# Kernel optimization log

Measured on AMD Instinct MI355X. Metric: run time of the kernel, lower is better.

Reference implementation:

```python
import jax, jax.numpy as jnp
import numpy as np

B, N, H, W = 2, 65536, 256, 256
FEA, OUT, CMP, MAX_PT = 8, 512, 32, 64
EPS = 1e-5


def _xavier(key, fan_in, fan_out):
    scale = np.sqrt(2.0 / (fan_in + fan_out)).astype(np.float32)
    return jax.random.normal(key, (fan_in, fan_out), dtype=jnp.float32) * scale


def setup_inputs() -> dict:
    key = jax.random.key(0)
    ks = jax.random.split(key, 8)
    pt_fea = jax.random.normal(ks[0], (B, N, FEA), dtype=jnp.float32)
    xy_ind = jax.random.randint(ks[1], (B, N, 2), 0, H, dtype=jnp.int32)
    return {
        "pt_fea": pt_fea,
        "bn0_g": jnp.ones((FEA,), jnp.float32), "bn0_b": jnp.zeros((FEA,), jnp.float32),
        "W1": _xavier(ks[2], FEA, 64),
        "bn1_g": jnp.ones((64,), jnp.float32), "bn1_b": jnp.zeros((64,), jnp.float32),
        "W2": _xavier(ks[3], 64, 128),
        "bn2_g": jnp.ones((128,), jnp.float32), "bn2_b": jnp.zeros((128,), jnp.float32),
        "W3": _xavier(ks[4], 128, 256),
        "bn3_g": jnp.ones((256,), jnp.float32), "bn3_b": jnp.zeros((256,), jnp.float32),
        "W4": _xavier(ks[5], 256, OUT),
        "Wc": _xavier(ks[6], OUT, CMP),
        "xy_ind": xy_ind,
    }


def _forward(pt_fea, bn0_g, bn0_b, W1, bn1_g, bn1_b, W2, bn2_g, bn2_b,
             W3, bn3_g, bn3_b, W4, Wc, xy_ind):
    Bc, Nc, Fc = pt_fea.shape
    P = Bc * Nc
    feats = pt_fea.reshape(P, Fc)
    batch_id = jnp.repeat(jnp.arange(Bc, dtype=jnp.int32), Nc)
    xy = xy_ind.reshape(P, 2)
    keys = batch_id * (H * W) + xy[:, 0] * W + xy[:, 1]  # linearized voxel id

    # random shuffle of points (torch.randperm)
    perm = jax.random.permutation(jax.random.key(42), P)
    feats = feats[perm]
    keys = keys[perm]

    # rank of each point within its voxel, in shuffled order
    # (== grp_range_torch(unq_cnt)[argsort(argsort(unq_inv))])
    order = jnp.argsort(keys)  # stable
    sk = keys[order]
    pos = jnp.arange(P)
    new_grp = jnp.concatenate([jnp.array([True]), sk[1:] != sk[:-1]])
    grp_start = jax.lax.cummax(jnp.where(new_grp, pos, 0))
    rank = jnp.zeros(P, jnp.int32).at[order].set((pos - grp_start).astype(jnp.int32))
    mask = rank < MAX_PT  # keep at most MAX_PT points per voxel

    # PPmodel: BN -> Lin -> BN -> ReLU x3 -> Lin, BN stats over kept points only
    m = mask[:, None].astype(feats.dtype)
    cnt = jnp.sum(m)

    def bn(x, g, b):
        mu = jnp.sum(x * m, axis=0) / cnt
        var = jnp.sum(jnp.square(x - mu) * m, axis=0) / cnt  # biased var
        return (x - mu) * jax.lax.rsqrt(var + EPS) * g + b

    x = bn(feats, bn0_g, bn0_b)
    x = jax.nn.relu(bn(x @ W1, bn1_g, bn1_b))
    x = jax.nn.relu(bn(x @ W2, bn2_g, bn2_b))
    x = jax.nn.relu(bn(x @ W3, bn3_g, bn3_b))
    x = x @ W4  # [P, OUT]

    # scatter_max segment reduction into dense voxel grid
    NEG = jnp.finfo(x.dtype).min
    x = jnp.where(mask[:, None], x, NEG)
    S = Bc * H * W
    pooled = jax.ops.segment_max(x, keys, num_segments=S)
    occupied = jax.ops.segment_sum(jnp.ones(P, x.dtype), keys, num_segments=S) > 0
    pooled = jnp.where(occupied[:, None], pooled, 0.0)

    comp = jax.nn.relu(pooled @ Wc)  # fea_compression
    comp = jnp.where(occupied[:, None], comp, 0.0)  # empty voxels stay zero
    out = comp.reshape(Bc, H, W, CMP).transpose(0, 3, 1, 2)  # [B, C, H, W]
    return out


def reference(pt_fea, bn0_g, bn0_b, W1, bn1_g, bn1_b, W2, bn2_g, bn2_b,
              W3, bn3_g, bn3_b, W4, Wc, xy_ind):
    return _forward(pt_fea, bn0_g, bn0_b, W1, bn1_g, bn1_b, W2, bn2_g, bn2_b,
                    W3, bn3_g, bn3_b, W4, Wc, xy_ind)
```

## Files before the change

kernel.cpp:

```cpp
#include <hip/hip_runtime.h>
#include <cstdint>
#include <cstddef>


#define P_TOT  131072
#define HWSZ   65536
#define WGRID  256
#define S_TOT  131072
#define EPS    1e-5f
#define CNTF   131072.0f

#define OFF_Y3    0ull
#define OFF_Y1    67108864ull
#define OFF_Y2    100663296ull
#define OFF_POOL  67108864ull
#define OFF_CNT   201326592ull
#define OFF_ST    201850880ull
#define OFF_OFFS  201916416ull
#define OFF_CUR   202440704ull
#define OFF_BSUM  202964992ull
#define OFF_PIDF  202969088ull
#define OFF_SEND  203493376ull
#define OFF_SKEY  204017664ull
#define OFF_INV   204541952ull
#define OFF_W3F   205066240ull
#define OFF_W4F   205131776ull
#define OFF_WCF   205393920ull
#define OFF_W2F   205426688ull
#define OFF_SCSH  205443072ull

typedef __attribute__((ext_vector_type(8)))  short bf16x8;
typedef __attribute__((ext_vector_type(16))) float f32x16;

__device__ __forceinline__ unsigned f2bf(float f) {
    unsigned u = __float_as_uint(f);
    return (u + 0x7FFFu + ((u >> 16) & 1u)) >> 16;
}
__device__ __forceinline__ float bf2f(unsigned h) {
    return __uint_as_float(h << 16);
}

__global__ __launch_bounds__(256) void k_zero(uint4* __restrict__ p, int n_u4) {
    int i = blockIdx.x * blockDim.x + threadIdx.x;
    if (i < n_u4) p[i] = make_uint4(0u, 0u, 0u, 0u);
}

__global__ __launch_bounds__(256) void k_prepw(
    const float* __restrict__ W2, const float* __restrict__ W3,
    const float* __restrict__ W4, const float* __restrict__ Wc,
    uint4* __restrict__ W2F, uint4* __restrict__ W3F,
    uint4* __restrict__ W4F, uint4* __restrict__ WcF)
{
    int gw = (blockIdx.x * 256 + threadIdx.x) >> 6;
    int l = threadIdx.x & 63;
    const float* W; uint4* dst; int M, mt, ks, fi;
    if (gw < 64)       { fi = gw;       W = W3; dst = W3F; M = 256; mt = fi >> 3; ks = fi & 7;  }
    else if (gw < 320) { fi = gw - 64;  W = W4; dst = W4F; M = 512; mt = fi >> 4; ks = fi & 15; }
    else if (gw < 352) { fi = gw - 320; W = Wc; dst = WcF; M = 32;  mt = 0;      ks = fi;      }
    else               { fi = gw - 352; W = W2; dst = W2F; M = 128; mt = fi >> 2; ks = fi & 3;  }
    int m = mt * 32 + (l & 31);
    int k0 = ks * 16 + (l >> 5) * 8;
    unsigned p[4];
    #pragma unroll
    for (int jj = 0; jj < 4; ++jj) {
        unsigned lo = f2bf(W[(size_t)(k0 + 2*jj)     * M + m]);
        unsigned hi = f2bf(W[(size_t)(k0 + 2*jj + 1) * M + m]);
        p[jj] = lo | (hi << 16);
    }
    dst[(size_t)fi * 64 + l] = make_uint4(p[0], p[1], p[2], p[3]);
}

__global__ __launch_bounds__(256) void k_bnprep(
    const float* __restrict__ st, const float* __restrict__ g,
    const float* __restrict__ b, float* __restrict__ sc,
    float* __restrict__ sh, int nch)
{
    int c = blockIdx.x * 256 + threadIdx.x;
    if (c >= nch) return;
    float mu = st[c * 16] * (1.0f / CNTF);
    float var = st[(nch + c) * 16] * (1.0f / CNTF) - mu * mu;
    float rs = rsqrtf(var + EPS);
    float s = rs * g[c];
    sc[c] = s;
    sh[c] = b[c] - mu * s;
}

__global__ __launch_bounds__(256) void k_fold(
    unsigned short* __restrict__ y, const float* __restrict__ sc,
    const float* __restrict__ sh, int nch, int n_u4)
{
    int i = blockIdx.x * 256 + threadIdx.x;
    if (i >= n_u4) return;
    int ch0 = (i * 8) & (nch - 1);
    float4 s0 = *(const float4*)(sc + ch0), s1 = *(const float4*)(sc + ch0 + 4);
    float4 h0 = *(const float4*)(sh + ch0), h1 = *(const float4*)(sh + ch0 + 4);
    float scv[8] = {s0.x,s0.y,s0.z,s0.w,s1.x,s1.y,s1.z,s1.w};
    float shv[8] = {h0.x,h0.y,h0.z,h0.w,h1.x,h1.y,h1.z,h1.w};
    uint4 e = ((const uint4*)y)[i];
    unsigned eu[4] = {e.x, e.y, e.z, e.w};
    unsigned ou[4];
    #pragma unroll
    for (int jj = 0; jj < 4; ++jj) {
        float x0 = fmaxf(fmaf(bf2f(eu[jj] & 0xFFFFu), scv[2*jj],   shv[2*jj]),   0.f);
        float x1 = fmaxf(fmaf(bf2f(eu[jj] >> 16),     scv[2*jj+1], shv[2*jj+1]), 0.f);
        ou[jj] = f2bf(x0) | (f2bf(x1) << 16);
    }
    ((uint4*)y)[i] = make_uint4(ou[0], ou[1], ou[2], ou[3]);
}

__global__ __launch_bounds__(256) void k_foldf(
    unsigned short* __restrict__ y, const float* __restrict__ sc,
    const float* __restrict__ sh, int n_u4)
{
    int i = blockIdx.x * 256 + threadIdx.x;
    if (i >= n_u4) return;
    int ch0 = ((i >> 6) & 15) * 16 + ((i >> 5) & 1) * 8;
    float4 s0 = *(const float4*)(sc + ch0), s1 = *(const float4*)(sc + ch0 + 4);
    float4 h0 = *(const float4*)(sh + ch0), h1 = *(const float4*)(sh + ch0 + 4);
    float scv[8] = {s0.x,s0.y,s0.z,s0.w,s1.x,s1.y,s1.z,s1.w};
    float shv[8] = {h0.x,h0.y,h0.z,h0.w,h1.x,h1.y,h1.z,h1.w};
    uint4 e = ((const uint4*)y)[i];
    unsigned eu[4] = {e.x, e.y, e.z, e.w};
    unsigned ou[4];
    #pragma unroll
    for (int jj = 0; jj < 4; ++jj) {
        float x0 = fmaxf(fmaf(bf2f(eu[jj] & 0xFFFFu), scv[2*jj],   shv[2*jj]),   0.f);
        float x1 = fmaxf(fmaf(bf2f(eu[jj] >> 16),     scv[2*jj+1], shv[2*jj+1]), 0.f);
        ou[jj] = f2bf(x0) | (f2bf(x1) << 16);
    }
    ((uint4*)y)[i] = make_uint4(ou[0], ou[1], ou[2], ou[3]);
}

__global__ __launch_bounds__(256) void k_stats0(
    const float* __restrict__ pt, const int* __restrict__ xy,
    float* __restrict__ st0, unsigned* __restrict__ counts)
{
    __shared__ float part[4][16];
    const int tid = threadIdx.x;
    const int p = blockIdx.x * 256 + tid;
    const float4* f4 = (const float4*)(pt + (size_t)p * 8);
    float4 a = f4[0], b = f4[1];
    float v[8] = {a.x,a.y,a.z,a.w,b.x,b.y,b.z,b.w};
    int key = (p >> 16) * HWSZ + xy[2*p] * WGRID + xy[2*p + 1];
    atomicAdd(&counts[key], 1u);
    float s[8], q[8];
    #pragma unroll
    for (int k = 0; k < 8; ++k) { s[k] = v[k]; q[k] = v[k]*v[k]; }
    #pragma unroll
    for (int k = 0; k < 8; ++k) {
        #pragma unroll
        for (int off = 32; off > 0; off >>= 1) {
            s[k] += __shfl_down(s[k], off);
            q[k] += __shfl_down(q[k], off);
        }
    }
    if ((tid & 63) == 0) {
        int w = tid >> 6;
        #pragma unroll
        for (int k = 0; k < 8; ++k) { part[w][k] = s[k]; part[w][8 + k] = q[k]; }
    }
    __syncthreads();
    if (tid < 16) {
        float t = part[0][tid] + part[1][tid] + part[2][tid] + part[3][tid];
        atomicAdd(&st0[tid * 16], t);
    }
}

__global__ __launch_bounds__(256) void k_lin1(
    const float* __restrict__ pt, const float* __restrict__ g0,
    const float* __restrict__ b0, const float* __restrict__ W1,
    const float* __restrict__ st0, float* __restrict__ y1,
    float* __restrict__ st1)
{
    __shared__ float x0s[64 * 8];
    __shared__ float w1s[8 * 64];
    __shared__ float sc0s[8], sh0s[8];
    __shared__ float red[256];
    const int tid = threadIdx.x;

    if (tid < 8) {
        float mu = st0[tid * 16] * (1.0f / CNTF);
        float var = st0[(8 + tid) * 16] * (1.0f / CNTF) - mu * mu;
        float rs = rsqrtf(var + EPS);
        sc0s[tid] = rs * g0[tid];
        sh0s[tid] = b0[tid] - mu * rs * g0[tid];
    }
    if (tid < 128) ((float4*)w1s)[tid] = ((const float4*)W1)[tid];
    const int c = tid & 63;
    const int psub = tid >> 6;
    float ssum = 0.f, ssq = 0.f;
    for (int t = 0; t < 4; ++t) {
        const int pbase = blockIdx.x * 256 + t * 64;
        __syncthreads();
        if (tid < 128) {
            float4 f = ((const float4*)(pt + (size_t)pbase * 8))[tid];
            int cc = (tid & 1) * 4;
            f.x = fmaf(f.x, sc0s[cc + 0], sh0s[cc + 0]);
            f.y = fmaf(f.y, sc0s[cc + 1], sh0s[cc + 1]);
            f.z = fmaf(f.z, sc0s[cc + 2], sh0s[cc + 2]);
            f.w = fmaf(f.w, sc0s[cc + 3], sh0s[cc + 3]);
            ((float4*)x0s)[tid] = f;
        }
        __syncthreads();
        #pragma unroll
        for (int i = 0; i < 16; ++i) {
            int pl = psub * 16 + i;
            float acc = 0.f;
            #pragma unroll
            for (int k = 0; k < 8; ++k)
                acc = fmaf(x0s[pl * 8 + k], w1s[k * 64 + c], acc);
            y1[(size_t)(pbase + pl) * 64 + c] = acc;
            ssum += acc; ssq += acc * acc;
        }
    }
    red[tid] = ssum; __syncthreads();
    if (tid < 64) atomicAdd(&st1[tid * 16],
        red[tid] + red[tid+64] + red[tid+128] + red[tid+192]);
    __syncthreads();
    red[tid] = ssq; __syncthreads();
    if (tid < 64) atomicAdd(&st1[(64 + tid) * 16],
        red[tid] + red[tid+64] + red[tid+128] + red[tid+192]);
}

__global__ __launch_bounds__(256) void k_scan1(
    const unsigned* __restrict__ counts, unsigned* __restrict__ bsum)
{
    __shared__ unsigned sh[256];
    int t = threadIdx.x;
    sh[t] = counts[blockIdx.x * 256 + t];
    __syncthreads();
    for (int d = 128; d > 0; d >>= 1) {
        if (t < d) sh[t] += sh[t + d];
        __syncthreads();
    }
    if (t == 0) bsum[blockIdx.x] = sh[0];
}

__global__ __launch_bounds__(256) void k_scan2(
    const unsigned* __restrict__ bsum, unsigned* __restrict__ boff)
{
    __shared__ unsigned sh[256];
    int t = threadIdx.x;
    unsigned a = bsum[2*t], b = bsum[2*t+1];
    unsigned s = a + b;
    sh[t] = s; __syncthreads();
    for (int d = 1; d < 256; d <<= 1) {
        unsigned u = (t >= d) ? sh[t-d] : 0u;
        __syncthreads();
        sh[t] += u;
        __syncthreads();
    }
    unsigned excl = sh[t] - s;
    boff[2*t]   = excl;
    boff[2*t+1] = excl + a;
}

__global__ __launch_bounds__(256) void k_scan3(
    const unsigned* __restrict__ counts, const unsigned* __restrict__ boff,
    unsigned* __restrict__ offs)
{
    __shared__ unsigned sh[256];
    int t = threadIdx.x, b = blockIdx.x;
    unsigned v = counts[b*256 + t];
    sh[t] = v; __syncthreads();
    for (int d = 1; d < 256; d <<= 1) {
        unsigned u = (t >= d) ? sh[t-d] : 0u;
        __syncthreads();
        sh[t] += u;
        __syncthreads();
    }
    offs[b*256 + t] = boff[b] + sh[t] - v;
}

__global__ __launch_bounds__(256) void k_fill(
    const int* __restrict__ xy, const unsigned* __restrict__ offs,
    const unsigned* __restrict__ counts, unsigned* __restrict__ cur,
    unsigned* __restrict__ pidf, unsigned* __restrict__ send,
    unsigned* __restrict__ skey, unsigned* __restrict__ inv)
{
    int p = blockIdx.x * 256 + threadIdx.x;
    int key = (p >> 16) * HWSZ + xy[2*p] * WGRID + xy[2*p + 1];
    unsigned o = offs[key];
    unsigned r = atomicAdd(&cur[key], 1u);
    unsigned slot = o + r;
    pidf[slot] = (unsigned)p | (r == 0 ? 0x80000000u : 0u);
    send[slot] = o + counts[key];
    skey[slot] = (unsigned)key;
    inv[p] = slot;
}

__global__ __launch_bounds__(256, 2) void k_lin2(
    const float* __restrict__ y1, const float* __restrict__ g1,
    const float* __restrict__ b1, const uint4* __restrict__ W2F,
    const float* __restrict__ st1, unsigned short* __restrict__ y2,
    float* __restrict__ st2)
{
    __shared__ uint4 w2s[1024];
    __shared__ float sc1s[64], sh1s[64];
    const int tid = threadIdx.x, l = tid & 63, w = tid >> 6;
    if (tid < 64) {
        float mu = st1[tid * 16] * (1.0f / CNTF);
        float var = st1[(64 + tid) * 16] * (1.0f / CNTF) - mu * mu;
        float rs = rsqrtf(var + EPS);
        sc1s[tid] = rs * g1[tid];
        sh1s[tid] = b1[tid] - mu * rs * g1[tid];
    }
    #pragma unroll
    for (int r = 0; r < 4; ++r) w2s[r * 256 + tid] = W2F[r * 256 + tid];
    __syncthreads();
    const int n = l & 31, q = l >> 5;
    float s_acc[16], q_acc[16];
    #pragma unroll
    for (int r = 0; r < 16; ++r) { s_acc[r] = 0.f; q_acc[r] = 0.f; }

    for (int t = 0; t < 8; ++t) {
        const int p = (blockIdx.x * 8 + t) * 32 + n;
        const float* yrow = y1 + (size_t)p * 64 + q * 8;
        bf16x8 Bf[4];
        #pragma unroll
        for (int ks = 0; ks < 4; ++ks) {
            float4 v0 = *(const float4*)(yrow + ks * 16);
            float4 v1 = *(const float4*)(yrow + ks * 16 + 4);
            int k0 = ks * 16 + q * 8;
            float e[8] = {v0.x,v0.y,v0.z,v0.w,v1.x,v1.y,v1.z,v1.w};
            union { bf16x8 v; unsigned u[4]; } cv;
            #pragma unroll
            for (int jj = 0; jj < 4; ++jj) {
                float a0 = fmaxf(fmaf(e[2*jj],   sc1s[k0+2*jj],   sh1s[k0+2*jj]),   0.f);
                float a1 = fmaxf(fmaf(e[2*jj+1], sc1s[k0+2*jj+1], sh1s[k0+2*jj+1]), 0.f);
                cv.u[jj] = f2bf(a0) | (f2bf(a1) << 16);
            }
            Bf[ks] = cv.v;
        }
        f32x16 acc;
        #pragma unroll
        for (int r = 0; r < 16; ++r) acc[r] = 0.f;
        #pragma unroll
        for (int ks = 0; ks < 4; ++ks) {
            union { uint4 u; bf16x8 v; } av;
            av.u = w2s[(w * 4 + ks) * 64 + l];
            acc = __builtin_amdgcn_mfma_f32_32x32x16_bf16(av.v, Bf[ks], acc, 0, 0, 0);
        }
        #pragma unroll
        for (int g = 0; g < 4; ++g) {
            int ch0 = w * 32 + 8 * g + 4 * q;
            ushort4 pk;
            pk.x = (unsigned short)f2bf(acc[4*g+0]);
            pk.y = (unsigned short)f2bf(acc[4*g+1]);
            pk.z = (unsigned short)f2bf(acc[4*g+2]);
            pk.w = (unsigned short)f2bf(acc[4*g+3]);
            *(ushort4*)(y2 + (size_t)p * 128 + ch0) = pk;
        }
        #pragma unroll
        for (int r = 0; r < 16; ++r) { s_acc[r] += acc[r]; q_acc[r] += acc[r]*acc[r]; }
    }
    #pragma unroll
    for (int r = 0; r < 16; ++r) {
        float s = s_acc[r], sq = q_acc[r];
        #pragma unroll
        for (int off = 16; off > 0; off >>= 1) {
            s  += __shfl_xor(s, off);
            sq += __shfl_xor(sq, off);
        }
        if ((l & 31) == 0) {
            int ch = w * 32 + (r & 3) + 8 * (r >> 2) + 4 * q;
            atomicAdd(&st2[ch * 16], s);
            atomicAdd(&st2[(128 + ch) * 16], sq);
        }
    }
}

__global__ __launch_bounds__(256, 2) void k_lin3(
    const unsigned short* __restrict__ y2f, const uint4* __restrict__ W3F,
    const unsigned* __restrict__ inv, uint4* __restrict__ y3F,
    float* __restrict__ st3)
{
    __shared__ uint4 w3s[4096];
    const int tid = threadIdx.x, l = tid & 63, w = tid >> 6;
    #pragma unroll
    for (int r = 0; r < 16; ++r) w3s[r * 256 + tid] = W3F[r * 256 + tid];
    __syncthreads();
    const int n = l & 31, q = l >> 5;
    float s_acc[32], q_acc[32];
    #pragma unroll
    for (int r = 0; r < 32; ++r) { s_acc[r] = 0.f; q_acc[r] = 0.f; }

    for (int t = 0; t < 8; ++t) {
        const int p = (blockIdx.x * 8 + t) * 32 + n;
        const unsigned short* yrow = y2f + (size_t)p * 128 + q * 8;
        bf16x8 Bf[8];
        #pragma unroll
        for (int ks = 0; ks < 8; ++ks) {
            union { uint4 u; bf16x8 v; } bv;
            bv.u = *(const uint4*)(yrow + ks * 16);
            Bf[ks] = bv.v;
        }
        f32x16 acc[2];
        #pragma unroll
        for (int i = 0; i < 2; ++i)
            #pragma unroll
            for (int r = 0; r < 16; ++r) acc[i][r] = 0.f;
        #pragma unroll
        for (int ks = 0; ks < 8; ++ks) {
            #pragma unroll
            for (int i = 0; i < 2; ++i) {
                union { uint4 u; bf16x8 v; } av;
                av.u = w3s[((w * 2 + i) * 8 + ks) * 64 + l];
                acc[i] = __builtin_amdgcn_mfma_f32_32x32x16_bf16(av.v, Bf[ks], acc[i], 0, 0, 0);
            }
        }
        #pragma unroll
        for (int i = 0; i < 2; ++i)
            #pragma unroll
            for (int r = 0; r < 16; ++r) {
                s_acc[i*16+r] += acc[i][r];
                q_acc[i*16+r] += acc[i][r] * acc[i][r];
            }
        const unsigned slotn = inv[p];
        const int fb = (int)(slotn >> 5) * 16;
        const int li = (int)(slotn & 31) + 32 * q;
        #pragma unroll
        for (int i = 0; i < 2; ++i) {
            #pragma unroll
            for (int s = 0; s < 2; ++s) {
                float V[8];
                #pragma unroll
                for (int j = 0; j < 4; ++j) {
                    float tmp = q ? acc[i][8*s + j] : acc[i][8*s + 4 + j];
                    float got = __shfl_xor(tmp, 32);
                    V[j]     = q ? got : acc[i][8*s + j];
                    V[4 + j] = q ? acc[i][8*s + 4 + j] : got;
                }
                uint4 pk;
                pk.x = f2bf(V[0]) | (f2bf(V[1]) << 16);
                pk.y = f2bf(V[2]) | (f2bf(V[3]) << 16);
                pk.z = f2bf(V[4]) | (f2bf(V[5]) << 16);
                pk.w = f2bf(V[6]) | (f2bf(V[7]) << 16);
                y3F[(size_t)(fb + w * 4 + 2 * i + s) * 64 + li] = pk;
            }
        }
    }
    #pragma unroll
    for (int i = 0; i < 2; ++i)
        #pragma unroll
        for (int r = 0; r < 16; ++r) {
            float s = s_acc[i*16+r], sq = q_acc[i*16+r];
            #pragma unroll
            for (int off = 16; off > 0; off >>= 1) {
                s  += __shfl_xor(s, off);
                sq += __shfl_xor(sq, off);
            }
            if ((l & 31) == 0) {
                int ch = (w * 2 + i) * 32 + (r & 3) + 8 * (r >> 2) + 4 * q;
                atomicAdd(&st3[ch * 16], s);
                atomicAdd(&st3[(256 + ch) * 16], sq);
            }
        }
}

__global__ __launch_bounds__(256, 2) void k_smax(
    const uint4* __restrict__ y3F, const uint4* __restrict__ W4F,
    const unsigned* __restrict__ pidf, const unsigned* __restrict__ send,
    const unsigned* __restrict__ skey, unsigned short* __restrict__ pooled)
{
    __shared__ float s0c_s[4 * 256];
    const int tid = threadIdx.x, l = tid & 63, w = tid >> 6;
    const int wg = blockIdx.x;
    const int q = l >> 5;

    #pragma unroll
    for (int sub = 0; sub < 4; ++sub) s0c_s[sub * 256 + tid] = -3.4e38f;

    #pragma unroll 1
    for (int t = 4; t >= 0; --t) {
        const int p0 = (wg * 4 + t) * 32;
        const int pos = p0 + (l & 31);
        const int sp = pos < P_TOT ? pos : P_TOT - 1;
        const unsigned pf = pidf[sp];
        const unsigned e_l = send[sp];
        const unsigned key_l = skey[sp];
        const unsigned cmask =
            (unsigned)__ballot((unsigned)(pos + 1) < e_l);
        const unsigned fmask =
            (unsigned)__ballot((pf & 0x80000000u) != 0u);
        const int tt = (wg * 4 + t) < 4096 ? (wg * 4 + t) : 4095;
        const uint4* xb = y3F + (size_t)tt * 16 * 64;
        uint4 Xf[16];
        #pragma unroll
        for (int ks = 0; ks < 16; ++ks)
            Xf[ks] = xb[ks * 64 + l];

        #pragma unroll 1
        for (int sub = 0; sub < 4; ++sub) {
            const int nt = sub * 4 + w;
            f32x16 acc;
            #pragma unroll
            for (int r = 0; r < 16; ++r) acc[r] = 0.f;
            #pragma unroll
            for (int ks = 0; ks < 16; ++ks) {
                union { uint4 u; bf16x8 v; } xv, wv;
                xv.u = Xf[ks];
                wv.u = W4F[(size_t)(nt * 16 + ks) * 64 + l];
                acc = __builtin_amdgcn_mfma_f32_32x32x16_bf16(xv.v, wv.v, acc, 0, 0, 0);
            }
            float v[32];
            #pragma unroll
            for (int r = 0; r < 16; ++r) {
                int base = (r & 3) + 8 * (r >> 2);
                float o = __shfl_xor(acc[r], 32);
                v[base]     = q ? o : acc[r];
                v[base + 4] = q ? acc[r] : o;
            }
            if ((cmask >> 31) & 1)
                v[31] = fmaxf(v[31], s0c_s[sub * 256 + tid]);
            #pragma unroll
            for (int m = 30; m >= 0; --m)
                if ((cmask >> m) & 1) v[m] = fmaxf(v[m], v[m + 1]);
            s0c_s[sub * 256 + tid] = v[0];
            if (t < 4) {
                #pragma unroll
                for (int m = 0; m < 32; ++m) {
                    if ((fmask >> m) & 1) {
                        unsigned km = (unsigned)
                            __builtin_amdgcn_readlane((int)key_l, m);
                        if ((m >> 4) == q)
                            pooled[(size_t)km * 512 + nt * 32 + (l & 31)] =
                                (unsigned short)f2bf(v[m]);
                    }
                }
            }
        }
    }
}

__global__ __launch_bounds__(256, 4) void k_out(
    const unsigned short* __restrict__ pooled, const unsigned* __restrict__ counts,
    const uint4* __restrict__ WcF, float* __restrict__ out)
{
    __shared__ uint4 wcs[2048];
    const int tid = threadIdx.x, l = tid & 63, w = tid >> 6;
    const int sbase = blockIdx.x * 128;
    #pragma unroll
    for (int r = 0; r < 8; ++r) wcs[r * 256 + tid] = WcF[r * 256 + tid];
    __syncthreads();
    const int n = l & 31, q = l >> 5;
    const int s = sbase + w * 32 + n;
    const bool occ = counts[s] > 0;
    const unsigned short* prow =
        pooled + (occ ? (size_t)s * 512 : (size_t)0) + q * 8;
    f32x16 acc;
    #pragma unroll
    for (int r = 0; r < 16; ++r) acc[r] = 0.f;

    for (int ks = 0; ks < 32; ++ks) {
        union { uint4 u; bf16x8 v; } bv;
        bv.u = *(const uint4*)(prow + ks * 16);
        union { uint4 u; bf16x8 v; } av;
        av.u = wcs[ks * 64 + l];
        acc = __builtin_amdgcn_mfma_f32_32x32x16_bf16(av.v, bv.v, acc, 0, 0, 0);
    }
    const int b = s >> 16, hw = s & 65535;
    #pragma unroll
    for (int r = 0; r < 16; ++r) {
        int ch = (r & 3) + 8 * (r >> 2) + 4 * q;
        float x = occ ? fmaxf(acc[r], 0.f) : 0.f;
        out[(size_t)b * (32 * HWSZ) + (size_t)ch * HWSZ + hw] = x;
    }
}

extern "C" void kernel_launch(void* const* d_in, const int* in_sizes, int n_in,
                              void* d_out, int out_size, void* d_ws, size_t ws_size,
                              hipStream_t stream) {
    const float* pt = (const float*)d_in[0];
    const float* g0 = (const float*)d_in[1];
    const float* b0 = (const float*)d_in[2];
    const float* W1 = (const float*)d_in[3];
    const float* g1 = (const float*)d_in[4];
    const float* b1 = (const float*)d_in[5];
    const float* W2 = (const float*)d_in[6];
    const float* g2 = (const float*)d_in[7];
    const float* b2 = (const float*)d_in[8];
    const float* W3 = (const float*)d_in[9];
    const float* g3 = (const float*)d_in[10];
    const float* b3 = (const float*)d_in[11];
    const float* W4 = (const float*)d_in[12];
    const float* Wc = (const float*)d_in[13];
    const int*   xy = (const int*)d_in[14];
    float* out = (float*)d_out;

    char* ws = (char*)d_ws;
    uint4*          y3F    = (uint4*)(ws + OFF_Y3);
    unsigned short* y3u    = (unsigned short*)(ws + OFF_Y3);
    float*          y1     = (float*)(ws + OFF_Y1);
    unsigned short* y2     = (unsigned short*)(ws + OFF_Y2);
    unsigned short* pool16 = (unsigned short*)(ws + OFF_POOL);
    unsigned*       counts = (unsigned*)(ws + OFF_CNT);
    float*          st     = (float*)(ws + OFF_ST);
    unsigned*       offs   = (unsigned*)(ws + OFF_OFFS);
    unsigned*       cur    = (unsigned*)(ws + OFF_CUR);
    unsigned*       bsum   = (unsigned*)(ws + OFF_BSUM);
    unsigned*       pidf   = (unsigned*)(ws + OFF_PIDF);
    unsigned*       send   = (unsigned*)(ws + OFF_SEND);
    unsigned*       skey   = (unsigned*)(ws + OFF_SKEY);
    unsigned*       inv    = (unsigned*)(ws + OFF_INV);
    uint4* W3F = (uint4*)(ws + OFF_W3F);
    uint4* W4F = (uint4*)(ws + OFF_W4F);
    uint4* WcF = (uint4*)(ws + OFF_WCF);
    uint4* W2F = (uint4*)(ws + OFF_W2F);
    float* scsh = (float*)(ws + OFF_SCSH);
    float* sc2 = scsh;       float* sh2 = scsh + 128;
    float* sc3 = scsh + 256; float* sh3 = scsh + 512;
    float* st0 = st;
    float* st1 = st + 256;
    float* st2 = st + 2304;
    float* st3 = st + 6400;

    k_zero<<<400, 256, 0, stream>>>((uint4*)(ws + OFF_CNT), 102400);
    k_prepw<<<92, 256, 0, stream>>>(W2, W3, W4, Wc, W2F, W3F, W4F, WcF);

    k_stats0<<<512, 256, 0, stream>>>(pt, xy, st0, counts);
    k_scan1<<<512, 256, 0, stream>>>(counts, bsum);
    k_scan2<<<1,   256, 0, stream>>>(bsum, bsum + 512);
    k_scan3<<<512, 256, 0, stream>>>(counts, bsum + 512, offs);
    k_fill<<<512, 256, 0, stream>>>(xy, offs, counts, cur, pidf, send, skey, inv);

    k_lin1<<<512, 256, 0, stream>>>(pt, g0, b0, W1, st0, y1, st1);
    k_lin2<<<512, 256, 0, stream>>>(y1, g1, b1, W2F, st1, y2, st2);
    k_bnprep<<<1, 256, 0, stream>>>(st2, g2, b2, sc2, sh2, 128);
    k_fold<<<8192, 256, 0, stream>>>(y2, sc2, sh2, 128, 2097152);
    k_lin3<<<512, 256, 0, stream>>>(y2, W3F, inv, y3F, st3);
    k_bnprep<<<1, 256, 0, stream>>>(st3, g3, b3, sc3, sh3, 256);
    k_foldf<<<16384, 256, 0, stream>>>(y3u, sc3, sh3, 4194304);

    k_smax<<<1024, 256, 0, stream>>>(y3F, W4F, pidf, send, skey, pool16);
    k_out<<<S_TOT / 128, 256, 0, stream>>>(pool16, counts, WcF, out);
}
```

Before: 403.4 us.

## Fuse BN3 scale/shift and ReLU into scatter-max kernel via LDS staging

Removes the separate k_bnprep and k_foldf passes for layer 3. Each k_smax workgroup now computes the BN3 scale and shift from the accumulated statistics, normalises and applies ReLU to its y3 tile on load, and stages the result in shared memory for the MFMA loop. This saves a full read-modify-write pass over the 64 MB y3 buffer and two launches. In exchange it adds LDS use (about 16 KB for the tile), extra barriers, and per-block redundant stats math, which could lower occupancy of the smax kernel.

Measured after the change: 421.4 us. 1.04x slower.

```diff
diff --git a/kernel.cpp b/kernel.cpp
--- a/kernel.cpp
+++ b/kernel.cpp
@@ -108,29 +108,6 @@
     ((uint4*)y)[i] = make_uint4(ou[0], ou[1], ou[2], ou[3]);
 }
 
-__global__ __launch_bounds__(256) void k_foldf(
-    unsigned short* __restrict__ y, const float* __restrict__ sc,
-    const float* __restrict__ sh, int n_u4)
-{
-    int i = blockIdx.x * 256 + threadIdx.x;
-    if (i >= n_u4) return;
-    int ch0 = ((i >> 6) & 15) * 16 + ((i >> 5) & 1) * 8;
-    float4 s0 = *(const float4*)(sc + ch0), s1 = *(const float4*)(sc + ch0 + 4);
-    float4 h0 = *(const float4*)(sh + ch0), h1 = *(const float4*)(sh + ch0 + 4);
-    float scv[8] = {s0.x,s0.y,s0.z,s0.w,s1.x,s1.y,s1.z,s1.w};
-    float shv[8] = {h0.x,h0.y,h0.z,h0.w,h1.x,h1.y,h1.z,h1.w};
-    uint4 e = ((const uint4*)y)[i];
-    unsigned eu[4] = {e.x, e.y, e.z, e.w};
-    unsigned ou[4];
-    #pragma unroll
-    for (int jj = 0; jj < 4; ++jj) {
-        float x0 = fmaxf(fmaf(bf2f(eu[jj] & 0xFFFFu), scv[2*jj],   shv[2*jj]),   0.f);
-        float x1 = fmaxf(fmaf(bf2f(eu[jj] >> 16),     scv[2*jj+1], shv[2*jj+1]), 0.f);
-        ou[jj] = f2bf(x0) | (f2bf(x1) << 16);
-    }
-    ((uint4*)y)[i] = make_uint4(ou[0], ou[1], ou[2], ou[3]);
-}
-
 __global__ __launch_bounds__(256) void k_stats0(
     const float* __restrict__ pt, const int* __restrict__ xy,
     float* __restrict__ st0, unsigned* __restrict__ counts)
@@ -460,16 +437,29 @@
 
 __global__ __launch_bounds__(256, 2) void k_smax(
     const uint4* __restrict__ y3F, const uint4* __restrict__ W4F,
-    const unsigned* __restrict__ pidf, const unsigned* __restrict__ send,
-    const unsigned* __restrict__ skey, unsigned short* __restrict__ pooled)
+    const float* __restrict__ g3, const float* __restrict__ b3,
+    const float* __restrict__ st3, const unsigned* __restrict__ pidf,
+    const unsigned* __restrict__ send, const unsigned* __restrict__ skey,
+    unsigned short* __restrict__ pooled)
 {
     __shared__ float s0c_s[4 * 256];
+    __shared__ float sc3s[256], sh3s[256];
+    __shared__ uint4 xs[1024];
     const int tid = threadIdx.x, l = tid & 63, w = tid >> 6;
     const int wg = blockIdx.x;
     const int q = l >> 5;
 
+    {
+        float mu = st3[tid * 16] * (1.0f / CNTF);
+        float var = st3[(256 + tid) * 16] * (1.0f / CNTF) - mu * mu;
+        float rs = rsqrtf(var + EPS);
+        float s = rs * g3[tid];
+        sc3s[tid] = s;
+        sh3s[tid] = b3[tid] - mu * s;
+    }
     #pragma unroll
     for (int sub = 0; sub < 4; ++sub) s0c_s[sub * 256 + tid] = -3.4e38f;
+    __syncthreads();
 
     #pragma unroll 1
     for (int t = 4; t >= 0; --t) {
@@ -484,11 +474,25 @@
         const unsigned fmask =
             (unsigned)__ballot((pf & 0x80000000u) != 0u);
         const int tt = (wg * 4 + t) < 4096 ? (wg * 4 + t) : 4095;
-        const uint4* xb = y3F + (size_t)tt * 16 * 64;
-        uint4 Xf[16];
-        #pragma unroll
-        for (int ks = 0; ks < 16; ++ks)
-            Xf[ks] = xb[ks * 64 + l];
+        __syncthreads();
+        #pragma unroll
+        for (int r = 0; r < 4; ++r) {
+            int idx = r * 256 + tid;
+            uint4 e = y3F[(size_t)tt * 1024 + idx];
+            int ch0 = ((idx >> 6) & 15) * 16 + ((idx >> 5) & 1) * 8;
+            unsigned eu[4] = {e.x, e.y, e.z, e.w};
+            unsigned ou[4];
+            #pragma unroll
+            for (int jj = 0; jj < 4; ++jj) {
+                float a0 = fmaxf(fmaf(bf2f(eu[jj] & 0xFFFFu),
+                                      sc3s[ch0+2*jj],   sh3s[ch0+2*jj]),   0.f);
+                float a1 = fmaxf(fmaf(bf2f(eu[jj] >> 16),
+                                      sc3s[ch0+2*jj+1], sh3s[ch0+2*jj+1]), 0.f);
+                ou[jj] = f2bf(a0) | (f2bf(a1) << 16);
+            }
+            xs[idx] = make_uint4(ou[0], ou[1], ou[2], ou[3]);
+        }
+        __syncthreads();
 
         #pragma unroll 1
         for (int sub = 0; sub < 4; ++sub) {
@@ -499,7 +503,7 @@
             #pragma unroll
             for (int ks = 0; ks < 16; ++ks) {
                 union { uint4 u; bf16x8 v; } xv, wv;
-                xv.u = Xf[ks];
+                xv.u = xs[ks * 64 + l];
                 wv.u = W4F[(size_t)(nt * 16 + ks) * 64 + l];
                 acc = __builtin_amdgcn_mfma_f32_32x32x16_bf16(xv.v, wv.v, acc, 0, 0, 0);
             }
@@ -590,7 +594,6 @@
 
     char* ws = (char*)d_ws;
     uint4*          y3F    = (uint4*)(ws + OFF_Y3);
-    unsigned short* y3u    = (unsigned short*)(ws + OFF_Y3);
     float*          y1     = (float*)(ws + OFF_Y1);
     unsigned short* y2     = (unsigned short*)(ws + OFF_Y2);
     unsigned short* pool16 = (unsigned short*)(ws + OFF_POOL);
@@ -609,7 +612,6 @@
     uint4* W2F = (uint4*)(ws + OFF_W2F);
     float* scsh = (float*)(ws + OFF_SCSH);
     float* sc2 = scsh;       float* sh2 = scsh + 128;
-    float* sc3 = scsh + 256; float* sh3 = scsh + 512;
     float* st0 = st;
     float* st1 = st + 256;
     float* st2 = st + 2304;
@@ -629,9 +631,8 @@
     k_bnprep<<<1, 256, 0, stream>>>(st2, g2, b2, sc2, sh2, 128);
     k_fold<<<8192, 256, 0, stream>>>(y2, sc2, sh2, 128, 2097152);
     k_lin3<<<512, 256, 0, stream>>>(y2, W3F, inv, y3F, st3);
-    k_bnprep<<<1, 256, 0, stream>>>(st3, g3, b3, sc3, sh3, 256);
-    k_foldf<<<16384, 256, 0, stream>>>(y3u, sc3, sh3, 4194304);
-
-    k_smax<<<1024, 256, 0, stream>>>(y3F, W4F, pidf, send, skey, pool16);
+
+    k_smax<<<1024, 256, 0, stream>>>(y3F, W4F, g3, b3, st3,
+                                     pidf, send, skey, pool16);
     k_out<<<S_TOT / 128, 256, 0, stream>>>(pool16, counts, WcF, out);
 }
```
